# Kernel tuning notes

Measured on AMD Instinct MI355X. Metric: run time of the kernel, lower is better.

## Reference

```python
import jax, jax.numpy as jnp
import numpy as np

B, N = 8192, 200  # batch of patches, fixed 200 points per patch


def setup_inputs() -> dict:
    key = jax.random.key(0)
    k1, = jax.random.split(key, 1)
    network_in = jax.random.normal(k1, (B, N, 13), dtype=jnp.float32)
    # learned parameters per build(): outward_shift init 0.25, a init 1, b init 0
    outward_shift = jnp.full((1,), 0.25, dtype=jnp.float32)
    a = jnp.ones((1,), dtype=jnp.float32)
    b = jnp.zeros((1,), dtype=jnp.float32)
    return {"network_in": network_in, "outward_shift": outward_shift, "a": a, "b": b}


def reference(network_in, outward_shift, a, b):
    w = network_in[:, :, 0:1]          # [B,N,1]
    xyz1 = network_in[:, :, 1:4]
    xyz2 = network_in[:, :, 4:7]       # also orig_xyz2
    norm1 = network_in[:, :, 7:10]
    norm2 = network_in[:, :, 10:13]

    w = jax.nn.relu(a * w + b) + 1e-8  # [B,N,1]

    v1 = xyz1 + norm1 * outward_shift
    v2 = xyz2 + norm2 * outward_shift

    w_sum = jnp.sum(w, axis=1)                       # [B,1]
    v1_ctr = jnp.sum(v1 * w, axis=1) / w_sum         # [B,3]
    v2_ctr = jnp.sum(v2 * w, axis=1) / w_sum         # [B,3]
    v1 = v1 - v1_ctr[:, None, :]
    v2 = v2 - v2_ctr[:, None, :]

    # cov = v2^T diag(w) v1, done without materializing the NxN diagonal
    cov = jnp.einsum('bni,bn,bnj->bij', v2, w[:, :, 0], v1)  # [B,3,3]

    # tf.linalg.svd: cov = u diag(s) v^T  ->  jnp svd: cov = u diag(s) vh, v = vh^T
    u, s, vh = jnp.linalg.svd(cov)
    v = jnp.swapaxes(vh, -1, -2)

    VUt = jnp.einsum('bik,bjk->bij', v, u)           # v @ u^T
    det_VUt = jnp.linalg.det(VUt)                    # [B]
    ones = jnp.ones_like(det_VUt)
    d = jnp.stack([ones, ones, det_VUt], axis=-1)    # [B,3]

    # R = v @ diag([1,1,det]) @ u^T
    R = jnp.einsum('bik,bk,bjk->bij', v, d, u)       # [B,3,3]

    t = v1_ctr - jnp.einsum('bij,bj->bi', R, v2_ctr) # [B,3]
    new_coords = jnp.einsum('bij,bnj->bni', R, xyz2) + t[:, None, :]
    return new_coords
```

## Files before the change

kernel.cpp:

```cpp
#include <hip/hip_runtime.h>
#include <math.h>

#define NPTS 200
#define NCH  13
#define BLK  256
#define FPB  (NPTS * NCH)

typedef float f4u __attribute__((ext_vector_type(4), aligned(4)));

typedef struct { float x, y, z; } f3s;

#define ACCUMULATE(Q0,Q1,Q2,Q3,Q4,Q5,Q6,Q7,Q8,Q9,Q10,Q11,Q12)               \
    {                                                                        \
        float wt = aa * (Q0) + bb;                                           \
        wt = fmaxf(wt, 0.f) + 1e-8f;                                         \
        const float v1x = fmaf(shift, (Q7),  (Q1));                          \
        const float v1y = fmaf(shift, (Q8),  (Q2));                          \
        const float v1z = fmaf(shift, (Q9),  (Q3));                          \
        const float v2x = fmaf(shift, (Q10), (Q4));                          \
        const float v2y = fmaf(shift, (Q11), (Q5));                          \
        const float v2z = fmaf(shift, (Q12), (Q6));                          \
        const float wv2x = wt * v2x, wv2y = wt * v2y, wv2z = wt * v2z;       \
        acc[0] += wt;                                                        \
        acc[1] += wt * v1x; acc[2] += wt * v1y; acc[3] += wt * v1z;          \
        acc[4] += wv2x;     acc[5] += wv2y;     acc[6] += wv2z;              \
        acc[7]  += wv2x * v1x; acc[8]  += wv2x * v1y; acc[9]  += wv2x * v1z; \
        acc[10] += wv2y * v1x; acc[11] += wv2y * v1y; acc[12] += wv2y * v1z; \
        acc[13] += wv2z * v1x; acc[14] += wv2z * v1y; acc[15] += wv2z * v1z; \
    }

#define ROTB(dp, dq, opq, e1p, e1q, e2p, e2q, P, Q)                          \
    {                                                                        \
        const float apq = opq;                                               \
        const float tau = (dq - dp) * 0.5f * __builtin_amdgcn_rcpf(apq);     \
        float tt = copysignf(1.0f, tau) * __builtin_amdgcn_rcpf(             \
                     fabsf(tau) +                                            \
                     __builtin_amdgcn_sqrtf(fmaf(tau, tau, 1.0f)));          \
        tt = (apq != 0.0f) ? tt : 0.0f;                                      \
        const float c = __builtin_amdgcn_rsqf(fmaf(tt, tt, 1.0f));           \
        const float s = tt * c;                                              \
        dp -= tt * apq;                                                      \
        dq += tt * apq;                                                      \
        opq = 0.0f;                                                          \
        { const float t1 = e1p; e1p = c * t1 - s * e1q;                      \
          e1q = s * t1 + c * e1q; }                                          \
        { const float t2 = e2p; e2p = c * t2 - s * e2q;                      \
          e2q = s * t2 + c * e2q; }                                          \
        _Pragma("unroll")                                                    \
        for (int k = 0; k < 4; ++k) {                                        \
            const float a1 = Vm[k][P], a2 = Vm[k][Q];                        \
            Vm[k][P] = c * a1 - s * a2;                                      \
            Vm[k][Q] = s * a1 + c * a2;                                      \
        }                                                                    \
    }

__global__ __launch_bounds__(BLK, 2) void fused_kernel(
    const float* __restrict__ net_in,
    const float* __restrict__ shift_p,
    const float* __restrict__ a_p,
    const float* __restrict__ b_p,
    float* __restrict__ out)
{
    const int tid = threadIdx.x;
    const int w   = tid >> 6;
    const int l   = tid & 63;
    const int t   = l & 15;
    const int b   = (blockIdx.x * 4 + w) * 4 + (l >> 4);

    const float shift = shift_p[0];
    const float aa    = a_p[0];
    const float bb    = b_p[0];

    const float* src = net_in + (size_t)b * FPB;

    float acc[16];
    #pragma unroll
    for (int k = 0; k < 16; ++k) acc[k] = 0.f;

    float sx2[13], sy2[13], sz2[13];

    #pragma unroll
    for (int i = 0; i < 13; ++i) {
        if (i < 12 || t < 8) {
            const float* q = src + (t + 16 * i) * NCH;
            const f4u v0 = *(const f4u*)(q);
            const f4u v1 = *(const f4u*)(q + 4);
            const f4u v2 = *(const f4u*)(q + 8);
            const float q12 = q[12];
            ACCUMULATE(v0.x, v0.y, v0.z, v0.w,
                       v1.x, v1.y, v1.z, v1.w,
                       v2.x, v2.y, v2.z, v2.w, q12)
            sx2[i] = v1.x; sy2[i] = v1.y; sz2[i] = v1.z;
        } else {
            sx2[i] = 0.f; sy2[i] = 0.f; sz2[i] = 0.f;
        }
    }

    #pragma unroll
    for (int k = 0; k < 16; ++k) {
        acc[k] += __shfl_xor(acc[k],  8, 64);
        acc[k] += __shfl_xor(acc[k],  4, 64);
        acc[k] += __shfl_xor(acc[k],  2, 64);
        acc[k] += __shfl_xor(acc[k],  1, 64);
    }

    const float W = acc[0];
    const float invW = __builtin_amdgcn_rcpf(W);
    const float v1cx = acc[1] * invW, v1cy = acc[2] * invW, v1cz = acc[3] * invW;
    const float v2cx = acc[4] * invW, v2cy = acc[5] * invW, v2cz = acc[6] * invW;

    const float Sxx = acc[7]  - W * v2cx * v1cx;
    const float Sxy = acc[8]  - W * v2cx * v1cy;
    const float Sxz = acc[9]  - W * v2cx * v1cz;
    const float Syx = acc[10] - W * v2cy * v1cx;
    const float Syy = acc[11] - W * v2cy * v1cy;
    const float Syz = acc[12] - W * v2cy * v1cz;
    const float Szx = acc[13] - W * v2cz * v1cx;
    const float Szy = acc[14] - W * v2cz * v1cy;
    const float Szz = acc[15] - W * v2cz * v1cz;

    float d0  = Sxx + Syy + Szz;
    float o01 = Syz - Szy;
    float o02 = Szx - Sxz;
    float o03 = Sxy - Syx;
    float d1  = Sxx - Syy - Szz;
    float o12 = Sxy + Syx;
    float o13 = Szx + Sxz;
    float d2  = -Sxx + Syy - Szz;
    float o23 = Syz + Szy;
    float d3  = -Sxx - Syy + Szz;

    float Vm[4][4] = {{1,0,0,0},{0,1,0,0},{0,0,1,0},{0,0,0,1}};

    for (int sweep = 0; sweep < 4; ++sweep) {
        ROTB(d0, d1, o01,  o02, o12,  o03, o13,  0, 1)
        ROTB(d0, d2, o02,  o01, o12,  o03, o23,  0, 2)
        ROTB(d0, d3, o03,  o01, o13,  o02, o23,  0, 3)
        ROTB(d1, d2, o12,  o01, o02,  o13, o23,  1, 2)
        ROTB(d1, d3, o13,  o01, o03,  o12, o23,  1, 3)
        ROTB(d2, d3, o23,  o02, o03,  o12, o13,  2, 3)
    }

    float bd = d0;
    float q0 = Vm[0][0], qx = Vm[1][0], qy = Vm[2][0], qz = Vm[3][0];
    { const bool c1 = d1 > bd;
      bd = c1 ? d1 : bd;
      q0 = c1 ? Vm[0][1] : q0; qx = c1 ? Vm[1][1] : qx;
      qy = c1 ? Vm[2][1] : qy; qz = c1 ? Vm[3][1] : qz; }
    { const bool c2 = d2 > bd;
      bd = c2 ? d2 : bd;
      q0 = c2 ? Vm[0][2] : q0; qx = c2 ? Vm[1][2] : qx;
      qy = c2 ? Vm[2][2] : qy; qz = c2 ? Vm[3][2] : qz; }
    { const bool c3 = d3 > bd;
      q0 = c3 ? Vm[0][3] : q0; qx = c3 ? Vm[1][3] : qx;
      qy = c3 ? Vm[2][3] : qy; qz = c3 ? Vm[3][3] : qz; }

    const float qn = __builtin_amdgcn_rsqf(q0*q0 + qx*qx + qy*qy + qz*qz);
    q0 *= qn; qx *= qn; qy *= qn; qz *= qn;

    const float R00 = q0*q0 + qx*qx - qy*qy - qz*qz;
    const float R01 = 2.0f * (qx*qy - q0*qz);
    const float R02 = 2.0f * (qx*qz + q0*qy);
    const float R10 = 2.0f * (qx*qy + q0*qz);
    const float R11 = q0*q0 - qx*qx + qy*qy - qz*qz;
    const float R12 = 2.0f * (qy*qz - q0*qx);
    const float R20 = 2.0f * (qx*qz - q0*qy);
    const float R21 = 2.0f * (qy*qz + q0*qx);
    const float R22 = q0*q0 - qx*qx - qy*qy + qz*qz;

    const float tx = v1cx - (R00 * v2cx + R01 * v2cy + R02 * v2cz);
    const float ty = v1cy - (R10 * v2cx + R11 * v2cy + R12 * v2cz);
    const float tz = v1cz - (R20 * v2cx + R21 * v2cy + R22 * v2cz);

    float* ob = out + (size_t)b * (NPTS * 3);
    #pragma unroll
    for (int i = 0; i < 13; ++i) {
        if (i < 12 || t < 8) {
            const int p = t + 16 * i;
            const float X = sx2[i], Y = sy2[i], Z = sz2[i];
            f3s o3;
            o3.x = R00 * X + R01 * Y + R02 * Z + tx;
            o3.y = R10 * X + R11 * Y + R12 * Z + ty;
            o3.z = R20 * X + R21 * Y + R22 * Z + tz;
            *(f3s*)(ob + p * 3) = o3;
        }
    }
}

extern "C" void kernel_launch(void* const* d_in, const int* in_sizes, int n_in,
                              void* d_out, int out_size, void* d_ws, size_t ws_size,
                              hipStream_t stream) {
    const float* net_in  = (const float*)d_in[0];
    const float* shift_p = (const float*)d_in[1];
    const float* a_p     = (const float*)d_in[2];
    const float* b_p     = (const float*)d_in[3];
    float* out = (float*)d_out;

    const int B = in_sizes[0] / FPB;
    (void)d_ws; (void)ws_size; (void)n_in; (void)out_size;

    fused_kernel<<<B / 16, BLK, 0, stream>>>(net_in, shift_p, a_p, b_p, out);
}
```

Baseline: 136.3 us.

## Stage half of each block's patches into LDS via direct global-to-LDS loads

Shrinks blocks to a single 64-thread wave handling four patches. The first two patches are bulk-copied into shared memory with global_load_lds and read from LDS, while the other two still load straight from global memory with unaligned vector loads. The aim is coalesced, wide transfers for part of the input without register staging. In exchange it adds a full waitcnt stall before any compute, leaves half the data on the old path, and puts about 20KB of LDS on each small block, which may limit occupancy.

```diff
diff --git a/kernel.cpp b/kernel.cpp
--- a/kernel.cpp
+++ b/kernel.cpp
@@ -3,8 +3,9 @@
 
 #define NPTS 200
 #define NCH  13
-#define BLK  256
+#define BLK  64
 #define FPB  (NPTS * NCH)
+#define STG  5200
 
 typedef float f4u __attribute__((ext_vector_type(4), aligned(4)));
 
@@ -41,7 +42,7 @@
         const float s = tt * c;                                              \
         dp -= tt * apq;                                                      \
         dq += tt * apq;                                                      \
-        opq = 0.0f;                                                          \
+        opq = 0.0f;                                                         \
         { const float t1 = e1p; e1p = c * t1 - s * e1q;                      \
           e1q = s * t1 + c * e1q; }                                          \
         { const float t2 = e2p; e2p = c * t2 - s * e2q;                      \
@@ -61,17 +62,36 @@
     const float* __restrict__ b_p,
     float* __restrict__ out)
 {
-    const int tid = threadIdx.x;
-    const int w   = tid >> 6;
-    const int l   = tid & 63;
-    const int t   = l & 15;
-    const int b   = (blockIdx.x * 4 + w) * 4 + (l >> 4);
+    __shared__ float s_in[STG];
+
+    const int l = threadIdx.x;
+    const int t = l & 15;
+    const int g = l >> 4;
+    const int b = blockIdx.x * 4 + g;
 
     const float shift = shift_p[0];
     const float aa    = a_p[0];
     const float bb    = b_p[0];
 
-    const float* src = net_in + (size_t)b * FPB;
+    const float* src  = net_in + (size_t)b * FPB;
+    const float* wsrc = net_in + (size_t)(blockIdx.x * 4) * FPB;
+
+    #pragma unroll
+    for (int j = 0; j < 20; ++j) {
+        __builtin_amdgcn_global_load_lds(
+            (const __attribute__((address_space(1))) void*)(wsrc + j * 256 + l * 4),
+            (__attribute__((address_space(3))) void*)(s_in + j * 256),
+            16, 0, 0);
+    }
+    if (l < 20) {
+        __builtin_amdgcn_global_load_lds(
+            (const __attribute__((address_space(1))) void*)(wsrc + 5120 + l * 4),
+            (__attribute__((address_space(3))) void*)(s_in + 5120),
+            16, 0, 0);
+    }
+
+    __builtin_amdgcn_s_waitcnt(0);
+    __asm__ __volatile__("" ::: "memory");
 
     float acc[16];
     #pragma unroll
@@ -79,20 +99,38 @@
 
     float sx2[13], sy2[13], sz2[13];
 
-    #pragma unroll
-    for (int i = 0; i < 13; ++i) {
-        if (i < 12 || t < 8) {
-            const float* q = src + (t + 16 * i) * NCH;
-            const f4u v0 = *(const f4u*)(q);
-            const f4u v1 = *(const f4u*)(q + 4);
-            const f4u v2 = *(const f4u*)(q + 8);
-            const float q12 = q[12];
-            ACCUMULATE(v0.x, v0.y, v0.z, v0.w,
-                       v1.x, v1.y, v1.z, v1.w,
-                       v2.x, v2.y, v2.z, v2.w, q12)
-            sx2[i] = v1.x; sy2[i] = v1.y; sz2[i] = v1.z;
-        } else {
-            sx2[i] = 0.f; sy2[i] = 0.f; sz2[i] = 0.f;
+    if (g < 2) {
+        const float* base = s_in + g * FPB;
+        #pragma unroll
+        for (int i = 0; i < 13; ++i) {
+            if (i < 12 || t < 8) {
+                const float* q = base + (t + 16 * i) * NCH;
+                const float q0 = q[0],  q1 = q[1],  q2  = q[2],  q3  = q[3];
+                const float q4 = q[4],  q5 = q[5],  q6  = q[6],  q7  = q[7];
+                const float q8 = q[8],  q9 = q[9],  q10 = q[10], q11 = q[11];
+                const float q12 = q[12];
+                ACCUMULATE(q0, q1, q2, q3, q4, q5, q6, q7, q8, q9, q10, q11, q12)
+                sx2[i] = q4; sy2[i] = q5; sz2[i] = q6;
+            } else {
+                sx2[i] = 0.f; sy2[i] = 0.f; sz2[i] = 0.f;
+            }
+        }
+    } else {
+        #pragma unroll
+        for (int i = 0; i < 13; ++i) {
+            if (i < 12 || t < 8) {
+                const float* q = src + (t + 16 * i) * NCH;
+                const f4u v0 = *(const f4u*)(q);
+                const f4u v1 = *(const f4u*)(q + 4);
+                const f4u v2 = *(const f4u*)(q + 8);
+                const float q12 = q[12];
+                ACCUMULATE(v0.x, v0.y, v0.z, v0.w,
+                           v1.x, v1.y, v1.z, v1.w,
+                           v2.x, v2.y, v2.z, v2.w, q12)
+                sx2[i] = v1.x; sy2[i] = v1.y; sz2[i] = v1.z;
+            } else {
+                sx2[i] = 0.f; sy2[i] = 0.f; sz2[i] = 0.f;
+            }
         }
     }
 
@@ -199,5 +237,5 @@
     const int B = in_sizes[0] / FPB;
     (void)d_ws; (void)ws_size; (void)n_in; (void)out_size;
 
-    fused_kernel<<<B / 16, BLK, 0, stream>>>(net_in, shift_p, a_p, b_p, out);
+    fused_kernel<<<B / 4, BLK, 0, stream>>>(net_in, shift_p, a_p, b_p, out);
 }
```

New measurement: 139.8 us. 2.6% more time.
